# Optimization experiments

Hardware: AMD Instinct MI355X
Metric: run time of the kernel (lower is better)

## Reference

```python
import jax, jax.numpy as jnp
import numpy as np

S = 32            # state: nodes per graph, conv output channels
B = 4096          # number of graphs
N = B * S         # total nodes
E = 2 * 1024 * 1024  # total edges (avg degree 16)
A = 2             # action_space_dimension
NACT = 32         # number_of_actions (adv heads)
EPS = 1e-5


def setup_inputs() -> dict:
    key = jax.random.key(0)
    ks = jax.random.split(key, 24)
    f = lambda k, sh, s: (jax.random.normal(k, sh, jnp.float32) * s)
    return {
        'x': f(ks[0], (N, 2), 1.0),
        'edge_index': jax.random.randint(ks[1], (2, E), 0, N),
        # conv1 MLP: Linear(4,16) -> ReLU -> Linear(16,S)
        'c1W1': f(ks[2], (4, 16), 0.5), 'c1b1': jnp.zeros((16,), jnp.float32),
        'c1W2': f(ks[3], (16, S), 0.25), 'c1b2': jnp.zeros((S,), jnp.float32),
        # conv2/conv3 MLPs: Linear(2*S,16) -> ReLU -> Linear(16,S)
        'c2W1': f(ks[4], (2 * S, 16), 0.12), 'c2b1': jnp.zeros((16,), jnp.float32),
        'c2W2': f(ks[5], (16, S), 0.25), 'c2b2': jnp.zeros((S,), jnp.float32),
        'c3W1': f(ks[6], (2 * S, 16), 0.12), 'c3b1': jnp.zeros((16,), jnp.float32),
        'c3W2': f(ks[7], (16, S), 0.25), 'c3b2': jnp.zeros((S,), jnp.float32),
        # 3 BatchNorm1d(S) layers (stacked)
        'bn_g': jnp.ones((3, S), jnp.float32), 'bn_b': jnp.zeros((3, S), jnp.float32),
        # dense head MLP 1024->256->256->256
        'mW1': f(ks[8], (S * S, 256), 0.03), 'mb1': jnp.zeros((256,), jnp.float32),
        'mW2': f(ks[9], (256, 256), 0.06), 'mb2': jnp.zeros((256,), jnp.float32),
        'mW3': f(ks[10], (256, 256), 0.06), 'mb3': jnp.zeros((256,), jnp.float32),
        # dueling heads
        'vW': f(ks[11], (256, 1), 0.06), 'vb': jnp.zeros((1,), jnp.float32),
        'aW': f(ks[12], (NACT, 256, A), 0.06), 'ab': jnp.zeros((NACT, A), jnp.float32),
    }


def _edgeconv(x, src, dst, W1, b1, W2, b2):
    # PyG EdgeConv with aggr='add': msg = MLP(cat[x_i, x_j - x_i]), summed at target i
    xi = x[dst]                       # [E, F]
    xj = x[src]                       # [E, F]
    m = jnp.concatenate([xi, xj - xi], axis=-1)        # [E, 2F]
    h = jnp.maximum(m @ W1 + b1, 0.0) @ W2 + b2        # [E, S]
    return jax.ops.segment_sum(h, dst, num_segments=x.shape[0])  # [N, S]


def _bn(h, g, b):
    # BatchNorm1d in training mode: batch stats over node dim, biased variance
    mu = h.mean(axis=0)
    var = jnp.mean((h - mu) ** 2, axis=0)
    return (h - mu) * jax.lax.rsqrt(var + EPS) * g + b


def reference(x, edge_index, c1W1, c1b1, c1W2, c1b2, c2W1, c2b1, c2W2, c2b2,
              c3W1, c3b1, c3W2, c3b2, bn_g, bn_b, mW1, mb1, mW2, mb2,
              mW3, mb3, vW, vb, aW, ab):
    src, dst = edge_index[0], edge_index[1]
    h = _edgeconv(x, src, dst, c1W1, c1b1, c1W2, c1b2)
    h = jax.nn.relu(_bn(h, bn_g[0], bn_b[0]))
    h = _edgeconv(h, src, dst, c2W1, c2b1, c2W2, c2b2)
    h = jax.nn.relu(_bn(h, bn_g[1], bn_b[1]))
    h = _edgeconv(h, src, dst, c3W1, c3b1, c3W2, c3b2)
    h = jax.nn.relu(_bn(h, bn_g[2], bn_b[2]))
    nb = x.shape[0] // S                                 # graphs in batch
    out = h.reshape(nb, S * S)                           # [B, in_size]
    out = jax.nn.relu(out @ mW1 + mb1)
    out = jax.nn.relu(out @ mW2 + mb2)
    out = jax.nn.relu(out @ mW3 + mb3)                   # [B, 256]
    value = out @ vW + vb                                # [B, 1]
    adv = jnp.einsum('bf,nfa->bna', out, aW) + ab        # [B, NACT, A]
    q = value[:, :, None] + adv - adv.mean(axis=2, keepdims=True)
    return q
```

## Files before the change

### kernel.cpp

```cpp
#include <hip/hip_runtime.h>
#include <hip/hip_fp16.h>

#define NN 131072
#define EE 2097152
#define SS 32
#define HH 16
#define BB 4096
#define EPS 1e-5f

#define BKT 512
#define BNODES 256
#define CAP 4864
#define TILE 8192

typedef _Float16 f16x8 __attribute__((ext_vector_type(8)));
typedef float f32x4 __attribute__((ext_vector_type(4)));

__global__ __launch_bounds__(256) void k_bsort(const int* __restrict__ ei, int* __restrict__ gcount,
                                               int* __restrict__ words) {
    __shared__ int cnt[BKT];
    __shared__ int tstart[BKT];
    __shared__ int gshift[BKT];
    __shared__ int stmp[256];
    __shared__ int sword[TILE];
    __shared__ int sdst[TILE];
    int t = threadIdx.x;
    cnt[t] = 0;
    cnt[t + 256] = 0;
    __syncthreads();
    int e0 = blockIdx.x * TILE;
#pragma unroll
    for (int it = 0; it < TILE / 256; ++it) {
        int dst = ei[EE + e0 + it * 256 + t];
        atomicAdd(&cnt[dst >> 8], 1);
    }
    __syncthreads();
    int c0 = cnt[2 * t], c1 = cnt[2 * t + 1];
    int tot = c0 + c1;
    stmp[t] = tot;
    __syncthreads();
    for (int d = 1; d < 256; d <<= 1) {
        int v = (t >= d) ? stmp[t - d] : 0;
        __syncthreads();
        stmp[t] += v;
        __syncthreads();
    }
    int excl = stmp[t] - tot;
    tstart[2 * t] = excl;
    tstart[2 * t + 1] = excl + c0;
    gshift[2 * t]     = (2 * t) * CAP     + atomicAdd(&gcount[2 * t], c0) - excl;
    gshift[2 * t + 1] = (2 * t + 1) * CAP + atomicAdd(&gcount[2 * t + 1], c1) - (excl + c0);
    cnt[2 * t] = 0;
    cnt[2 * t + 1] = 0;
    __syncthreads();
#pragma unroll
    for (int it = 0; it < TILE / 256; ++it) {
        int e = e0 + it * 256 + t;
        int src = ei[e];
        int dst = ei[EE + e];
        int b = dst >> 8;
        int r = atomicAdd(&cnt[b], 1);
        int p = tstart[b] + r;
        sword[p] = src | ((dst & 255) << 17);
        sdst[p] = gshift[b] + p;
    }
    __syncthreads();
#pragma unroll
    for (int it = 0; it < TILE / 256; ++it) {
        int i = it * 256 + t;
        words[sdst[i]] = sword[i];
    }
}

__global__ __launch_bounds__(256) void k_csr(const int* __restrict__ words, const int* __restrict__ gcount,
                                             int* __restrict__ ssrc, int* __restrict__ offs,
                                             int* __restrict__ offe) {
    __shared__ int hist[BNODES];
    __shared__ int sc[BNODES];
    __shared__ int base[BNODES];
    int t = threadIdx.x;
    int b = blockIdx.x;
    hist[t] = 0;
    __syncthreads();
    int cnt = gcount[b];
    const int* wp = words + (size_t)b * CAP;
    for (int p = t; p < cnt; p += 256) atomicAdd(&hist[wp[p] >> 17], 1);
    __syncthreads();
    int val = hist[t];
    sc[t] = val;
    __syncthreads();
    for (int d = 1; d < 256; d <<= 1) {
        int v2 = (t >= d) ? sc[t - d] : 0;
        __syncthreads();
        sc[t] += v2;
        __syncthreads();
    }
    base[t] = sc[t] - val;
    int gbase = b * CAP;
    offs[b * BNODES + t] = gbase + base[t];
    offe[b * BNODES + t] = gbase + sc[t];
    __syncthreads();
    hist[t] = 0;
    __syncthreads();
    for (int p = t; p < cnt; p += 256) {
        int w = wp[p];
        int dl = w >> 17;
        int r = atomicAdd(&hist[dl], 1);
        ssrc[gbase + base[dl] + r] = w & 0x1FFFF;
    }
}

__global__ __launch_bounds__(256) void k_prep(const float* __restrict__ mW1, const float* __restrict__ mW2,
                                              const float* __restrict__ mW3, const float* __restrict__ vW,
                                              const float* __restrict__ vb, const float* __restrict__ aW,
                                              const float* __restrict__ ab,
                                              _Float16* __restrict__ W1T, _Float16* __restrict__ W2T,
                                              _Float16* __restrict__ W3T, _Float16* __restrict__ BqT,
                                              float* __restrict__ biasq, int* __restrict__ gcount,
                                              float* __restrict__ bns) {
    int i = blockIdx.x * 256 + threadIdx.x;
    {
        int k = i >> 8, n = i & 255;
        W1T[(size_t)n * 1024 + k] = (_Float16)mW1[i];
    }
    if (i < 65536) {
        int k = i >> 8, n = i & 255;
        W2T[n * 256 + k] = (_Float16)mW2[i];
        W3T[n * 256 + k] = (_Float16)mW3[i];
    }
    if (i < 16384) {
        int f = i >> 6, j = i & 63;
        int n = j >> 1, a = j & 1;
        float wa = aW[n * 512 + f * 2 + a];
        float wo = aW[n * 512 + f * 2 + (1 - a)];
        BqT[j * 256 + f] = (_Float16)(vW[f] + 0.5f * (wa - wo));
    }
    if (i < 64) biasq[i] = vb[0] + 0.5f * (ab[i] - ab[i ^ 1]);
    if (i < 512) gcount[i] = 0;
    if (i < 192) bns[i] = 0.f;
}

__global__ __launch_bounds__(256) void k_pre1(const float* __restrict__ x, const float* __restrict__ W1,
                                              const float* __restrict__ b1, float* __restrict__ u,
                                              __half* __restrict__ v) {
    int t = blockIdx.x * 256 + threadIdx.x;
    int n = t >> 4, c = t & 15;
    float x0 = x[n * 2], x1 = x[n * 2 + 1];
    float w0 = W1[c], w1 = W1[16 + c], w2 = W1[32 + c], w3 = W1[48 + c];
    u[t] = b1[c] + x0 * (w0 - w2) + x1 * (w1 - w3);
    v[t] = __float2half(x0 * w2 + x1 * w3);
    if (blockIdx.x == 0 && t < 16) v[NN * 16 + t] = __float2half(-60000.0f);
}

__global__ __launch_bounds__(256) void k_bnpre(const float* __restrict__ y, const float* __restrict__ bns,
                                               const float* __restrict__ g, const float* __restrict__ bb,
                                               const float* __restrict__ W1, const float* __restrict__ b1,
                                               float* __restrict__ u, __half* __restrict__ v) {
    __shared__ float sh[16][33];
    __shared__ float wd[32][16];
    __shared__ float wv[32][16];
    __shared__ float scL[32], soL[32];
    int t = threadIdx.x;
    if (t < 32) {
        const float inv_n = 1.0f / (float)NN;
        float mean = bns[t] * inv_n;
        float var = bns[32 + t] * inv_n - mean * mean;
        float s = g[t] * rsqrtf(var + EPS);
        scL[t] = s;
        soL[t] = bb[t] - mean * s;
    }
    for (int i = t; i < 512; i += 256) {
        int f = i >> 4, c = i & 15;
        float wt = W1[i];
        float wb = W1[512 + i];
        wd[f][c] = wt - wb;
        wv[f][c] = wb;
    }
    __syncthreads();
    int nb = blockIdx.x * 16;
    for (int i = t; i < 512; i += 256) {
        int col = i & 31;
        sh[i >> 5][col] = fmaxf(y[nb * 32 + i] * scL[col] + soL[col], 0.f);
    }
    __syncthreads();
    int c = t & 15, nl = t >> 4;
    float uu = b1[c], vv = 0.f;
#pragma unroll
    for (int f = 0; f < 32; ++f) {
        float hv = sh[nl][f];
        uu += hv * wd[f][c];
        vv += hv * wv[f][c];
    }
    int n = nb + nl;
    u[n * 16 + c] = uu;
    v[n * 16 + c] = __float2half(vv);
    if (blockIdx.x == 0 && t < 16) v[NN * 16 + t] = __float2half(-60000.0f);
}

__global__ __launch_bounds__(256) void k_gather(const float* __restrict__ u, const __half* __restrict__ v,
                                                const int* __restrict__ ssrc, const int* __restrict__ offs,
                                                const int* __restrict__ offe,
                                                const float* __restrict__ W2, const float* __restrict__ b2,
                                                float* __restrict__ y) {
    __shared__ float sw2[512];
    __shared__ float sagg[32 * 18];
    __shared__ float cntL[32];
    int t = threadIdx.x;
    float w2a = W2[t], w2b = W2[t + 256];
    float b2r0 = b2[(t & 7) * 4], b2r1 = b2[(t & 7) * 4 + 1];
    float b2r2 = b2[(t & 7) * 4 + 2], b2r3 = b2[(t & 7) * 4 + 3];
    int nl = t >> 3, c2 = t & 7;
    int n = blockIdx.x * 32 + nl;
    int s0 = offs[n], e0 = offe[n];
    float2 uc = *(const float2*)(u + (size_t)n * 16 + 2 * c2);
    float a0 = 0.f, a1 = 0.f;
    for (int p = s0; p < e0; p += 16) {
        int idx[16];
#pragma unroll
        for (int i = 0; i < 16; ++i) idx[i] = (p + i < e0) ? ssrc[p + i] : NN;
        float2 vv[16];
#pragma unroll
        for (int i = 0; i < 16; ++i)
            vv[i] = __half22float2(*(const __half2*)(v + (size_t)idx[i] * 16 + 2 * c2));
#pragma unroll
        for (int i = 0; i < 16; ++i) {
            a0 += fmaxf(uc.x + vv[i].x, 0.f);
            a1 += fmaxf(uc.y + vv[i].y, 0.f);
        }
    }
    sagg[nl * 18 + 2 * c2] = a0;
    sagg[nl * 18 + 2 * c2 + 1] = a1;
    if (c2 == 0) cntL[nl] = (float)(e0 - s0);
    sw2[t] = w2a;
    sw2[t + 256] = w2b;
    __syncthreads();
    int node = t >> 3, oc = (t & 7) * 4;
    float cw = cntL[node];
    float o0 = b2r0 * cw, o1 = b2r1 * cw, o2 = b2r2 * cw, o3 = b2r3 * cw;
#pragma unroll
    for (int k = 0; k < 16; ++k) {
        float a = sagg[node * 18 + k];
        o0 += a * sw2[k * 32 + oc];
        o1 += a * sw2[k * 32 + oc + 1];
        o2 += a * sw2[k * 32 + oc + 2];
        o3 += a * sw2[k * 32 + oc + 3];
    }
    *(float4*)(y + (size_t)(blockIdx.x * 32 + node) * 32 + oc) = make_float4(o0, o1, o2, o3);
}

__global__ __launch_bounds__(256) void k_bnstat2(const float* __restrict__ y, float* __restrict__ bns) {
    __shared__ float ssm[8][33];
    __shared__ float ssq[8][33];
    int t = threadIdx.x;
    int c = t & 31, g = t >> 5;
    size_t r0 = (size_t)blockIdx.x * 512;
    float sm = 0.f, sq = 0.f;
    for (int i = 0; i < 64; ++i) {
        float val = y[(r0 + g + (size_t)i * 8) * 32 + c];
        sm += val;
        sq += val * val;
    }
    ssm[g][c] = sm;
    ssq[g][c] = sq;
    __syncthreads();
    if (t < 32) {
        float a = 0.f, bq = 0.f;
#pragma unroll
        for (int gg = 0; gg < 8; ++gg) { a += ssm[gg][t]; bq += ssq[gg][t]; }
        atomicAdd(&bns[t], a);
        atomicAdd(&bns[32 + t], bq);
    }
}

__global__ __launch_bounds__(256) void k_bnrelu16(const float* __restrict__ y, const float* __restrict__ bns,
                                                  const float* __restrict__ g, const float* __restrict__ bb,
                                                  _Float16* __restrict__ h16) {
    int t = blockIdx.x * 256 + threadIdx.x;
    int j = t & 31;
    const float inv_n = 1.0f / (float)NN;
    float mean = bns[j] * inv_n;
    float var = bns[32 + j] * inv_n - mean * mean;
    float sc = g[j] * rsqrtf(var + EPS);
    float sh = bb[j] - mean * sc;
    h16[t] = (_Float16)fmaxf(y[t] * sc + sh, 0.f);
}

__global__ __launch_bounds__(256) void k_mgemm(const _Float16* __restrict__ A, const _Float16* __restrict__ BT,
                                               const float* __restrict__ bias, float* __restrict__ Cf,
                                               _Float16* __restrict__ Ch, int M, int N, int K,
                                               int relu, int out16) {
    int tid = threadIdx.x;
    int w = tid >> 6, l = tid & 63, q = l >> 4, r = l & 15;
    int rowBase = blockIdx.x * 64;
    int col = blockIdx.y * 64 + w * 16 + r;
    const _Float16* ap = A + (size_t)(rowBase + r) * K + q * 8;
    const _Float16* bp = BT + (size_t)col * K + q * 8;
    f32x4 z = {0.f, 0.f, 0.f, 0.f};
    f32x4 acc[4] = {z, z, z, z};
    for (int k0 = 0; k0 < K; k0 += 32) {
        f16x8 bf = *(const f16x8*)(bp + k0);
        f16x8 a0 = *(const f16x8*)(ap + k0);
        f16x8 a1 = *(const f16x8*)(ap + k0 + (size_t)16 * K);
        f16x8 a2 = *(const f16x8*)(ap + k0 + (size_t)32 * K);
        f16x8 a3 = *(const f16x8*)(ap + k0 + (size_t)48 * K);
        acc[0] = __builtin_amdgcn_mfma_f32_16x16x32_f16(a0, bf, acc[0], 0, 0, 0);
        acc[1] = __builtin_amdgcn_mfma_f32_16x16x32_f16(a1, bf, acc[1], 0, 0, 0);
        acc[2] = __builtin_amdgcn_mfma_f32_16x16x32_f16(a2, bf, acc[2], 0, 0, 0);
        acc[3] = __builtin_amdgcn_mfma_f32_16x16x32_f16(a3, bf, acc[3], 0, 0, 0);
    }
    float bv = bias[col];
#pragma unroll
    for (int rt = 0; rt < 4; ++rt) {
#pragma unroll
        for (int i = 0; i < 4; ++i) {
            int row = rowBase + rt * 16 + q * 4 + i;
            float val = acc[rt][i] + bv;
            if (relu) val = fmaxf(val, 0.f);
            if (out16) Ch[(size_t)row * N + col] = (_Float16)val;
            else       Cf[(size_t)row * N + col] = val;
        }
    }
}

extern "C" void kernel_launch(void* const* d_in, const int* in_sizes, int n_in,
                              void* d_out, int out_size, void* d_ws, size_t ws_size,
                              hipStream_t stream) {
    const float* x    = (const float*)d_in[0];
    const int*   ei   = (const int*)d_in[1];
    const float* c1W1 = (const float*)d_in[2];
    const float* c1b1 = (const float*)d_in[3];
    const float* c1W2 = (const float*)d_in[4];
    const float* c1b2 = (const float*)d_in[5];
    const float* c2W1 = (const float*)d_in[6];
    const float* c2b1 = (const float*)d_in[7];
    const float* c2W2 = (const float*)d_in[8];
    const float* c2b2 = (const float*)d_in[9];
    const float* c3W1 = (const float*)d_in[10];
    const float* c3b1 = (const float*)d_in[11];
    const float* c3W2 = (const float*)d_in[12];
    const float* c3b2 = (const float*)d_in[13];
    const float* bn_g = (const float*)d_in[14];
    const float* bn_b = (const float*)d_in[15];
    const float* mW1  = (const float*)d_in[16];
    const float* mb1  = (const float*)d_in[17];
    const float* mW2  = (const float*)d_in[18];
    const float* mb2  = (const float*)d_in[19];
    const float* mW3  = (const float*)d_in[20];
    const float* mb3  = (const float*)d_in[21];
    const float* vW   = (const float*)d_in[22];
    const float* vb   = (const float*)d_in[23];
    const float* aW   = (const float*)d_in[24];
    const float* ab   = (const float*)d_in[25];
    float* out = (float*)d_out;

    char* p = (char*)d_ws;
    auto take = [&](size_t bytes) {
        char* r = p;
        p += (bytes + 255) & ~(size_t)255;
        return r;
    };
    int*       gcount = (int*)take((size_t)BKT * 4);
    int*       words  = (int*)take((size_t)BKT * CAP * 4);
    int*       ssrc   = (int*)take((size_t)BKT * CAP * 4);
    int*       offs   = (int*)take((size_t)NN * 4);
    int*       offe   = (int*)take((size_t)NN * 4);
    float*     u      = (float*)take((size_t)NN * HH * 4);
    __half*    v      = (__half*)take((size_t)(NN + 1) * HH * 2);
    float*     y      = (float*)take((size_t)NN * SS * 4);
    _Float16*  h16    = (_Float16*)take((size_t)NN * SS * 2);
    float*     bns    = (float*)take(3 * 64 * 4);
    _Float16*  W1T    = (_Float16*)take((size_t)256 * 1024 * 2);
    _Float16*  W2T    = (_Float16*)take((size_t)256 * 256 * 2);
    _Float16*  W3T    = (_Float16*)take((size_t)256 * 256 * 2);
    _Float16*  BqT    = (_Float16*)take((size_t)64 * 256 * 2);
    float*     biasq  = (float*)take(64 * 4);
    _Float16*  Xa     = (_Float16*)take((size_t)BB * 256 * 2);
    _Float16*  Xb     = (_Float16*)take((size_t)BB * 256 * 2);

    k_prep<<<1024, 256, 0, stream>>>(mW1, mW2, mW3, vW, vb, aW, ab,
                                     W1T, W2T, W3T, BqT, biasq, gcount, bns);

    k_bsort<<<EE / TILE, 256, 0, stream>>>(ei, gcount, words);
    k_csr<<<BKT, 256, 0, stream>>>(words, gcount, ssrc, offs, offe);

    k_pre1<<<NN * 16 / 256, 256, 0, stream>>>(x, c1W1, c1b1, u, v);
    k_gather<<<NN / 32, 256, 0, stream>>>(u, v, ssrc, offs, offe, c1W2, c1b2, y);
    k_bnstat2<<<256, 256, 0, stream>>>(y, bns);
    k_bnpre<<<NN / 16, 256, 0, stream>>>(y, bns, bn_g, bn_b, c2W1, c2b1, u, v);
    k_gather<<<NN / 32, 256, 0, stream>>>(u, v, ssrc, offs, offe, c2W2, c2b2, y);
    k_bnstat2<<<256, 256, 0, stream>>>(y, bns + 64);
    k_bnpre<<<NN / 16, 256, 0, stream>>>(y, bns + 64, bn_g + 32, bn_b + 32, c3W1, c3b1, u, v);
    k_gather<<<NN / 32, 256, 0, stream>>>(u, v, ssrc, offs, offe, c3W2, c3b2, y);
    k_bnstat2<<<256, 256, 0, stream>>>(y, bns + 128);
    k_bnrelu16<<<NN * 32 / 256, 256, 0, stream>>>(y, bns + 128, bn_g + 64, bn_b + 64, h16);

    k_mgemm<<<dim3(BB / 64, 4), 256, 0, stream>>>(h16, W1T, mb1, nullptr, Xa, BB, 256, 1024, 1, 1);
    k_mgemm<<<dim3(BB / 64, 4), 256, 0, stream>>>(Xa, W2T, mb2, nullptr, Xb, BB, 256, 256, 1, 1);
    k_mgemm<<<dim3(BB / 64, 4), 256, 0, stream>>>(Xb, W3T, mb3, nullptr, Xa, BB, 256, 256, 1, 1);
    k_mgemm<<<dim3(BB / 64, 1), 256, 0, stream>>>(Xa, BqT, biasq, out, nullptr, BB, 64, 256, 0, 0);
}
```

Measured before the change: 369.0 us.

## Pad per-node CSR segments to 16 and widen sort/CSR blocks

The CSR build now pads each destination node's source list up to a multiple of 16, filling the padding with a dummy index that points at a sentinel row, and uses a larger per-bucket capacity. This lets the gather kernel drop the per-element bounds check when loading indices. The bucket-sort kernel moves to 1024-thread blocks with a one-bucket-per-thread scan, and the CSR kernel moves to 512 threads. The trade-off is extra padding writes, a bigger ssrc buffer, and a serial padding loop per node.

```diff
diff --git a/kernel.cpp b/kernel.cpp
--- a/kernel.cpp
+++ b/kernel.cpp
@@ -11,51 +11,49 @@
 #define BKT 512
 #define BNODES 256
 #define CAP 4864
+#define SCAP 8192
 #define TILE 8192
 
 typedef _Float16 f16x8 __attribute__((ext_vector_type(8)));
 typedef float f32x4 __attribute__((ext_vector_type(4)));
 
-__global__ __launch_bounds__(256) void k_bsort(const int* __restrict__ ei, int* __restrict__ gcount,
-                                               int* __restrict__ words) {
+__global__ __launch_bounds__(1024) void k_bsort(const int* __restrict__ ei, int* __restrict__ gcount,
+                                                int* __restrict__ words) {
     __shared__ int cnt[BKT];
     __shared__ int tstart[BKT];
     __shared__ int gshift[BKT];
-    __shared__ int stmp[256];
+    __shared__ int sc[BKT];
     __shared__ int sword[TILE];
     __shared__ int sdst[TILE];
     int t = threadIdx.x;
-    cnt[t] = 0;
-    cnt[t + 256] = 0;
+    if (t < BKT) cnt[t] = 0;
     __syncthreads();
     int e0 = blockIdx.x * TILE;
 #pragma unroll
-    for (int it = 0; it < TILE / 256; ++it) {
-        int dst = ei[EE + e0 + it * 256 + t];
+    for (int it = 0; it < TILE / 1024; ++it) {
+        int dst = ei[EE + e0 + it * 1024 + t];
         atomicAdd(&cnt[dst >> 8], 1);
     }
     __syncthreads();
-    int c0 = cnt[2 * t], c1 = cnt[2 * t + 1];
-    int tot = c0 + c1;
-    stmp[t] = tot;
-    __syncthreads();
-    for (int d = 1; d < 256; d <<= 1) {
-        int v = (t >= d) ? stmp[t - d] : 0;
+    int val = (t < BKT) ? cnt[t] : 0;
+    if (t < BKT) sc[t] = val;
+    __syncthreads();
+    for (int d = 1; d < BKT; d <<= 1) {
+        int v2 = (t >= d && t < BKT) ? sc[t - d] : 0;
         __syncthreads();
-        stmp[t] += v;
+        if (t < BKT) sc[t] += v2;
         __syncthreads();
     }
-    int excl = stmp[t] - tot;
-    tstart[2 * t] = excl;
-    tstart[2 * t + 1] = excl + c0;
-    gshift[2 * t]     = (2 * t) * CAP     + atomicAdd(&gcount[2 * t], c0) - excl;
-    gshift[2 * t + 1] = (2 * t + 1) * CAP + atomicAdd(&gcount[2 * t + 1], c1) - (excl + c0);
-    cnt[2 * t] = 0;
-    cnt[2 * t + 1] = 0;
-    __syncthreads();
-#pragma unroll
-    for (int it = 0; it < TILE / 256; ++it) {
-        int e = e0 + it * 256 + t;
+    if (t < BKT) {
+        int excl = sc[t] - val;
+        tstart[t] = excl;
+        gshift[t] = t * CAP + atomicAdd(&gcount[t], val) - excl;
+        cnt[t] = 0;
+    }
+    __syncthreads();
+#pragma unroll
+    for (int it = 0; it < TILE / 1024; ++it) {
+        int e = e0 + it * 1024 + t;
         int src = ei[e];
         int dst = ei[EE + e];
         int b = dst >> 8;
@@ -66,13 +64,13 @@
     }
     __syncthreads();
 #pragma unroll
-    for (int it = 0; it < TILE / 256; ++it) {
-        int i = it * 256 + t;
+    for (int it = 0; it < TILE / 1024; ++it) {
+        int i = it * 1024 + t;
         words[sdst[i]] = sword[i];
     }
 }
 
-__global__ __launch_bounds__(256) void k_csr(const int* __restrict__ words, const int* __restrict__ gcount,
+__global__ __launch_bounds__(512) void k_csr(const int* __restrict__ words, const int* __restrict__ gcount,
                                              int* __restrict__ ssrc, int* __restrict__ offs,
                                              int* __restrict__ offe) {
     __shared__ int hist[BNODES];
@@ -80,33 +78,42 @@
     __shared__ int base[BNODES];
     int t = threadIdx.x;
     int b = blockIdx.x;
-    hist[t] = 0;
+    if (t < BNODES) hist[t] = 0;
     __syncthreads();
     int cnt = gcount[b];
     const int* wp = words + (size_t)b * CAP;
-    for (int p = t; p < cnt; p += 256) atomicAdd(&hist[wp[p] >> 17], 1);
-    __syncthreads();
-    int val = hist[t];
-    sc[t] = val;
-    __syncthreads();
-    for (int d = 1; d < 256; d <<= 1) {
-        int v2 = (t >= d) ? sc[t - d] : 0;
+    for (int p = t; p < cnt; p += 512) atomicAdd(&hist[wp[p] >> 17], 1);
+    __syncthreads();
+    int val = 0, pval = 0;
+    if (t < BNODES) {
+        val = hist[t];
+        pval = (val + 15) & ~15;
+        sc[t] = pval;
+    }
+    __syncthreads();
+    for (int d = 1; d < BNODES; d <<= 1) {
+        int v2 = (t >= d && t < BNODES) ? sc[t - d] : 0;
         __syncthreads();
-        sc[t] += v2;
+        if (t < BNODES) sc[t] += v2;
         __syncthreads();
     }
-    base[t] = sc[t] - val;
-    int gbase = b * CAP;
-    offs[b * BNODES + t] = gbase + base[t];
-    offe[b * BNODES + t] = gbase + sc[t];
-    __syncthreads();
-    hist[t] = 0;
-    __syncthreads();
-    for (int p = t; p < cnt; p += 256) {
+    int gbase = b * SCAP;
+    if (t < BNODES) {
+        base[t] = sc[t] - pval;
+        offs[b * BNODES + t] = gbase + base[t];
+        offe[b * BNODES + t] = gbase + base[t] + val;
+        hist[t] = 0;
+    }
+    __syncthreads();
+    for (int p = t; p < cnt; p += 512) {
         int w = wp[p];
         int dl = w >> 17;
         int r = atomicAdd(&hist[dl], 1);
         ssrc[gbase + base[dl] + r] = w & 0x1FFFF;
+    }
+    if (t < BNODES) {
+        int s = gbase + base[t];
+        for (int i = val; i < pval; ++i) ssrc[s + i] = NN;
     }
 }
 
@@ -212,12 +219,13 @@
     int nl = t >> 3, c2 = t & 7;
     int n = blockIdx.x * 32 + nl;
     int s0 = offs[n], e0 = offe[n];
+    int pe = s0 + ((e0 - s0 + 15) & ~15);
     float2 uc = *(const float2*)(u + (size_t)n * 16 + 2 * c2);
     float a0 = 0.f, a1 = 0.f;
-    for (int p = s0; p < e0; p += 16) {
+    for (int p = s0; p < pe; p += 16) {
         int idx[16];
 #pragma unroll
-        for (int i = 0; i < 16; ++i) idx[i] = (p + i < e0) ? ssrc[p + i] : NN;
+        for (int i = 0; i < 16; ++i) idx[i] = ssrc[p + i];
         float2 vv[16];
 #pragma unroll
         for (int i = 0; i < 16; ++i)
@@ -361,7 +369,7 @@
     };
     int*       gcount = (int*)take((size_t)BKT * 4);
     int*       words  = (int*)take((size_t)BKT * CAP * 4);
-    int*       ssrc   = (int*)take((size_t)BKT * CAP * 4);
+    int*       ssrc   = (int*)take((size_t)BKT * SCAP * 4);
     int*       offs   = (int*)take((size_t)NN * 4);
     int*       offe   = (int*)take((size_t)NN * 4);
     float*     u      = (float*)take((size_t)NN * HH * 4);
@@ -380,8 +388,8 @@
     k_prep<<<1024, 256, 0, stream>>>(mW1, mW2, mW3, vW, vb, aW, ab,
                                      W1T, W2T, W3T, BqT, biasq, gcount, bns);
 
-    k_bsort<<<EE / TILE, 256, 0, stream>>>(ei, gcount, words);
-    k_csr<<<BKT, 256, 0, stream>>>(words, gcount, ssrc, offs, offe);
+    k_bsort<<<EE / TILE, 1024, 0, stream>>>(ei, gcount, words);
+    k_csr<<<BKT, 512, 0, stream>>>(words, gcount, ssrc, offs, offe);
 
     k_pre1<<<NN * 16 / 256, 256, 0, stream>>>(x, c1W1, c1b1, u, v);
     k_gather<<<NN / 32, 256, 0, stream>>>(u, v, ssrc, offs, offe, c1W2, c1b2, y);
```

Measured after the change: 333.5 us. 1.11x faster.
